# Kernel optimization log

Hardware: AMD Instinct MI355X
Metric: run time of the kernel (lower is better)

## Reference

```python
import jax, jax.numpy as jnp
import numpy as np
from jax.scipy.special import logsumexp

SIZE = 68          # DP length (self.size)
SSN = 8            # number of secondary-structure classes
C = SSN + 1        # states per step
S1 = SIZE + 1      # positions
BATCH = 256


def setup_inputs() -> dict:
    key = jax.random.key(0)
    k1, k2, k3, k4 = jax.random.split(key, 4)
    P = jax.random.normal(k1, (BATCH, 1, C, S1, S1), jnp.float32)
    Q = jax.random.normal(k2, (1, C, C, S1, S1), jnp.float32)
    pi = jax.random.normal(k3, (C,), jnp.float32)
    T = jnp.ones((1,), jnp.float32)
    ls = jax.random.randint(k4, (BATCH,), 0, S1, dtype=jnp.int32)
    return {"P": P, "Q": Q, "pi": pi, "T": T, "ls": ls}


def _max_alpha(P, Q, pi, T):
    # Viterbi-style max-plus recursion with logsumexp renormalization.
    b = P.shape[0]
    a0 = jnp.full((b, C, S1), -jnp.inf, P.dtype).at[:, :, 0].set(pi[None, :])
    n0 = logsumexp(a0, axis=(-1, -2), keepdims=True)      # (b,1,1)
    a0 = a0 - n0

    def step(carry, _):
        la, ln = carry                                    # (b,C,S1), (b,1,1)
        # broadcast sum over (b, c_prev, c_new, t_prev, t_new)
        M = P + T * Q + la[:, :, None, :, None]
        a = M.max(axis=(1, 3))                            # max over c_prev, t_prev -> (b,C,S1)
        n = ln + logsumexp(a, axis=(-1, -2), keepdims=True)
        a = a + ln - n
        return (a, n), (a, n)

    _, (a_seq, n_seq) = jax.lax.scan(step, (a0, n0), None, length=SIZE)
    a_all = jnp.concatenate([a0[None], a_seq], 0)          # (S1, b, C, S1) forward order
    n_all = jnp.concatenate([n0[None], n_seq], 0)          # (S1, b, 1, 1)
    # torch code stacks alpha REVERSED but norm in forward order, then adds
    alpha = a_all[::-1] + n_all
    return jnp.swapaxes(alpha, 0, 1)                       # (b, SIZE+1, C, S1)


def _backtrace(alpha, P, Q, T, ls):
    b = alpha.shape[0]
    Ps = P[:, 0]            # (b, C, S1, S1)
    Qs = Q[0]               # (C, C, S1, S1)
    bi = jnp.arange(b)
    c0 = jnp.full((b,), 3, jnp.int32)
    l0 = jnp.zeros((b,), jnp.int32)
    t0 = ls.astype(jnp.int32)

    def step(carry, a):
        c, l, t = carry
        Pterm = Ps[bi, c, :, t]                 # (b, S1)
        Qterm = Qs[c, :, :, t]                  # (b, C, S1)
        score = Pterm[:, None, :] + T * Qterm + a
        idx = jnp.argmax(score.reshape(b, -1), axis=-1).astype(jnp.int32)
        cn = idx // S1
        tn = idx % S1
        ln = tn - t
        return (cn, ln, tn), (cn, ln, tn)

    a_seq = jnp.swapaxes(alpha, 0, 1)[1:]       # (SIZE, b, C, S1)
    _, (cs, lss, ts) = jax.lax.scan(step, (c0, l0, t0), a_seq)
    c_all = jnp.concatenate([c0[None], cs], 0)[::-1]   # (SIZE+1, b)
    l_all = jnp.concatenate([l0[None], lss], 0)[::-1]
    t_all = jnp.concatenate([t0[None], ts], 0)[::-1]
    mp = jnp.swapaxes(jnp.stack([c_all, l_all, t_all], -1), 0, 1)  # (b, SIZE+1, 3)
    # shift length column: mp[:, :-1, 1] = mp[:, 1:, 1]; mp[:, -1, 1] = 0
    l_shift = jnp.concatenate([mp[:, 1:, 1], jnp.zeros((b, 1), jnp.int32)], 1)
    return mp.at[:, :, 1].set(l_shift)


def reference(P, Q, pi, T, ls):
    alpha = _max_alpha(P, Q, pi, T)
    max_pattern = _backtrace(alpha, P, Q, T, ls)
    return alpha, max_pattern
```

## Files before the change

### kernel.cpp

```cpp
#include <hip/hip_runtime.h>

#define C9     9
#define S1     69
#define JT     621
#define NBATCH 256
#define NSTEP  68
#define QJ     4761
#define QI     42849
#define BROW   42849
#define ALPHA_N (NBATCH*BROW)
#define QTFL   385664
#define NEGINF (-__builtin_inff())

typedef float float4u __attribute__((ext_vector_type(4), aligned(4)));

__global__ void qw_kernel(const float* __restrict__ Q, float* __restrict__ QW)
{
  const int bl = blockIdx.x;
  const int j = bl / S1, s = bl - j*S1;
  float* dst = QW + (size_t)bl*JT;
  const float* src = Q + (size_t)j*QJ + s*S1;
  for (int f = threadIdx.x; f < JT; f += 256){
    const int i = f / S1, t = f - i*S1;
    dst[f] = src[i*QJ + t];
  }
}

__global__ void qtrans_kernel(const float* __restrict__ Q, float* __restrict__ QT)
{
  __shared__ float tile[69*70];
  const int pl = blockIdx.x;
  const int c = pl / 9, i = pl - c*9;
  const float* src = Q + (size_t)pl*QJ;
  for (int f = threadIdx.x; f < QJ; f += 256){
    const int s = f / S1, t = f - s*S1;
    tile[s*70 + t] = src[f];
  }
  __syncthreads();
  float* dst = QT + (size_t)c*QI + i*S1;
  for (int f = threadIdx.x; f < QJ; f += 256){
    const int t = f / S1, s = f - t*S1;
    dst[t*JT + s] = tile[s*70 + t];
  }
}

template<int SI, int SS>
__device__ __forceinline__ float4u scan12(const float* __restrict__ qb,
                                          const float* __restrict__ pb,
                                          const float* __restrict__ laS,
                                          const float Tv)
{
#define LD(BUF, PV, S) { \
  const float* q_ = qb + (S)*SS; \
  _Pragma("unroll") \
  for (int i_ = 0; i_ < C9; ++i_) BUF[i_] = *(const float4u*)(q_ + i_*SI); \
  PV = *(const float4u*)(pb + (S)*S1); }
#define CM(BUF, PV, S) { \
  float r0=NEGINF, r1=NEGINF, r2=NEGINF, r3=NEGINF; \
  _Pragma("unroll") \
  for (int i_ = 0; i_ < C9; ++i_){ \
    const float lv_ = laS[i_*72 + (S)]; \
    r0 = fmaxf(r0, fmaf(Tv, BUF[i_].x, lv_)); \
    r1 = fmaxf(r1, fmaf(Tv, BUF[i_].y, lv_)); \
    r2 = fmaxf(r2, fmaf(Tv, BUF[i_].z, lv_)); \
    r3 = fmaxf(r3, fmaf(Tv, BUF[i_].w, lv_)); \
  } \
  acc.x = fmaxf(acc.x, PV.x + r0); acc.y = fmaxf(acc.y, PV.y + r1); \
  acc.z = fmaxf(acc.z, PV.z + r2); acc.w = fmaxf(acc.w, PV.w + r3); }

  float4u acc; acc.x = acc.y = acc.z = acc.w = NEGINF;
  float4u qA[C9], qB[C9], pA, pB;
  int s = 0;
  LD(qA, pA, s)
  for (; s + 2 < 12; s += 2){
    LD(qB, pB, s+1)
    CM(qA, pA, s)
    LD(qA, pA, s+2)
    CM(qB, pB, s+1)
  }
  LD(qB, pB, s+1)
  CM(qA, pA, s)
  CM(qB, pB, s+1)
  return acc;
#undef LD
#undef CM
}

__global__ __launch_bounds__(1024, 4) void mega_kernel(
    const float* __restrict__ P, const float* __restrict__ Q,
    const float* __restrict__ pi, const float* __restrict__ Tp,
    const int* __restrict__ ls, float* __restrict__ out,
    const float* __restrict__ QW, const float* __restrict__ QT, int wsmode)
{
  __shared__ __align__(16) float la[2][C9*72];
  __shared__ float part[5][162][4];
  __shared__ float red[16];
  __shared__ float m_sh[NSTEP+1], lse_sh[NSTEP+1], n_sh[NSTEP+1];
  __shared__ float sums_sh[NSTEP+1][3];
  __shared__ float sbest[16];
  __shared__ int   sidx[16];
  __shared__ int   sct[2];

  const int tid  = threadIdx.x;
  const int w    = tid >> 6;
  const int lane = tid & 63;
  const int b    = blockIdx.x;
  const bool act = tid < 972;
  const int gg   = act ? tid / 162 : 5;
  const int slot = act ? tid - gg*162 : 0;
  const int j    = slot / 18;
  const int tq   = slot - j*18;
  const int t0   = (tq < 17) ? 4*tq : 65;
  const int s_lo = (gg*23) >> 1;
  const float Tv = Tp[0];

  float* outb = out + (size_t)b*BROW;

  for (int e = tid; e < JT; e += 1024){
    const int i = e / S1, s = e - i*S1;
    const float v0 = (s == 0) ? pi[i] : NEGINF;
    outb[68*JT + e] = v0;
    la[0][i*72 + s] = v0;
  }
  if (tid == 0){
    float mx = pi[0];
    #pragma unroll
    for (int c = 1; c < C9; ++c) mx = fmaxf(mx, pi[c]);
    float sm = 0.f;
    #pragma unroll
    for (int c = 0; c < C9; ++c) sm += expf(pi[c] - mx);
    m_sh[0]   = mx;
    lse_sh[0] = mx + logf(sm);
  }
  __syncthreads();
  float mprev = m_sh[0];

  const bool useQW = (wsmode >= 1);
  const float* qw_b = QW + (size_t)j*QI + (size_t)s_lo*JT + t0;
  const float* qr_b = Q + (size_t)j*QJ + s_lo*S1 + t0;
  const float* p_b  = P + (size_t)(b*C9 + j)*QJ + s_lo*S1 + t0;

  int cur = 0;
  for (int k = 1; k <= NSTEP; ++k){
    const float* laS = la[cur] + s_lo;
    float4u acc;
    if (act){
      if (useQW) acc = scan12<S1, JT>(qw_b, p_b, laS, Tv);
      else       acc = scan12<QI, S1>(qr_b, p_b, laS, Tv);
      if (gg > 0){
        part[gg-1][slot][0] = acc.x; part[gg-1][slot][1] = acc.y;
        part[gg-1][slot][2] = acc.z; part[gg-1][slot][3] = acc.w;
      }
    }
    __syncthreads();

    float mval = NEGINF;
    float v0 = 0.f, v1 = 0.f, v2 = 0.f, v3 = 0.f;
    if (act && gg == 0){
      float c0 = acc.x, c1 = acc.y, c2 = acc.z, c3 = acc.w;
      #pragma unroll
      for (int g = 0; g < 5; ++g){
        c0 = fmaxf(c0, part[g][slot][0]);
        c1 = fmaxf(c1, part[g][slot][1]);
        c2 = fmaxf(c2, part[g][slot][2]);
        c3 = fmaxf(c3, part[g][slot][3]);
      }
      v0 = c0 - mprev; v1 = c1 - mprev; v2 = c2 - mprev; v3 = c3 - mprev;
      float* dst = outb + (size_t)(68-k)*JT + j*S1 + t0;
      if (tq < 17){
        float4u vv; vv.x = v0; vv.y = v1; vv.z = v2; vv.w = v3;
        *(float4u*)dst = vv;
        *(float4*)(&la[cur^1][j*72 + t0]) = make_float4(v0, v1, v2, v3);
        mval = fmaxf(fmaxf(v0, v1), fmaxf(v2, v3));
      } else {
        dst[3] = v3;
        la[cur^1][j*72 + 68] = v3;
        mval = v3;
      }
    }
    float mr = mval;
    #pragma unroll
    for (int o = 32; o >= 1; o >>= 1) mr = fmaxf(mr, __shfl_down(mr, o));
    if (lane == 0) red[w] = mr;
    __syncthreads();
    const float mA = fmaxf(fmaxf(red[0], red[1]), red[2]);
    if (act && gg == 0){
      float sv = (tq < 17)
        ? expf(v0 - mA) + expf(v1 - mA) + expf(v2 - mA) + expf(v3 - mA)
        : expf(v3 - mA);
      #pragma unroll
      for (int o = 32; o >= 1; o >>= 1) sv += __shfl_down(sv, o);
      if (lane == 0) sums_sh[k][w] = sv;
    }
    if (tid == 0) m_sh[k] = mA;
    mprev = mA;
    cur ^= 1;
  }
  __syncthreads();

  if (tid == 0){
    double dd = 0.0;
    for (int kk = 0; kk <= NSTEP; ++kk){
      float lse;
      if (kk == 0) lse = lse_sh[0];
      else lse = m_sh[kk] + logf(sums_sh[kk][0] + sums_sh[kk][1] + sums_sh[kk][2]);
      lse_sh[kk] = lse;
      n_sh[kk] = (float)((double)lse + dd);
      dd += (double)m_sh[kk];
    }
  }
  __syncthreads();

  for (int K = 0; K <= NSTEP; ++K){
    const float Cst = n_sh[K] - lse_sh[68-K];
    for (int e = tid; e < JT; e += 1024){
      float* r = outb + (size_t)K*JT + e;
      *r = fmaxf(*r + Cst, -3.0e38f);
    }
  }
  __syncthreads();

  {
    int c = 3, t2 = ls[b];
    float* mpb = out + (size_t)ALPHA_N + (size_t)b*(69*3);
    if (tid == 0){
      mpb[68*3+0] = 3.f; mpb[68*3+1] = 0.f; mpb[68*3+2] = (float)t2;
      mpb[67*3+1] = 0.f;
    }
    const bool vok = tid < JT;
    const int etid = vok ? tid : 0;
    const int im = etid / S1;
    const int sm = etid - im*S1;
    float av = vok ? outb[1*JT + tid] : NEGINF;
    for (int r = 1; r <= NSTEP; ++r){
      float avn = NEGINF;
      if (r < NSTEP && vok) avn = outb[(size_t)(r+1)*JT + tid];
      float best = NEGINF; int bidx = 0x7fffffff;
      if (vok){
        float qv;
        if (wsmode >= 2)      qv = QT[(size_t)c*QI + (size_t)t2*JT + tid];
        else if (wsmode == 1) qv = QW[(size_t)c*QI + (size_t)sm*JT + im*S1 + t2];
        else                  qv = Q[(size_t)c*QI + (size_t)im*QJ + sm*S1 + t2];
        const float pv = P[(size_t)(b*C9 + c)*QJ + sm*S1 + t2];
        best = (pv + Tv*qv) + av;
        bidx = tid;
      }
      #pragma unroll
      for (int o = 32; o >= 1; o >>= 1){
        const float ov = __shfl_down(best, o); const int oi = __shfl_down(bidx, o);
        if (ov > best || (ov == best && oi < bidx)){ best = ov; bidx = oi; }
      }
      if (lane == 0){ sbest[w] = best; sidx[w] = bidx; }
      __syncthreads();
      if (tid == 0){
        float bb = sbest[0]; int bi = sidx[0];
        #pragma unroll
        for (int q = 1; q < 16; ++q)
          if (sbest[q] > bb || (sbest[q] == bb && sidx[q] < bi)){
            bb = sbest[q]; bi = sidx[q];
          }
        const int cn = bi / S1, tn = bi - cn*S1;
        mpb[(68-r)*3 + 0] = (float)cn;
        mpb[(68-r)*3 + 2] = (float)tn;
        if (r <= 67) mpb[(67-r)*3 + 1] = (float)(tn - t2);
        sct[0] = cn; sct[1] = tn;
      }
      __syncthreads();
      c = sct[0]; t2 = sct[1];
      av = avn;
    }
  }
}

extern "C" void kernel_launch(void* const* d_in, const int* in_sizes, int n_in,
                              void* d_out, int out_size, void* d_ws, size_t ws_size,
                              hipStream_t stream)
{
  const float* P  = (const float*)d_in[0];
  const float* Q  = (const float*)d_in[1];
  const float* pi = (const float*)d_in[2];
  const float* T  = (const float*)d_in[3];
  const int*   ls = (const int*)d_in[4];

  float* out = (float*)d_out;

  int wsmode = 0; float* QW = nullptr; float* QT = nullptr;
  if (ws_size >= (size_t)QTFL*4){ wsmode = 1; QW = (float*)d_ws; }
  if (ws_size >= (size_t)2*QTFL*4){ wsmode = 2; QT = (float*)d_ws + QTFL; }

  if (wsmode >= 1) qw_kernel<<<JT, 256, 0, stream>>>(Q, QW);
  if (wsmode >= 2) qtrans_kernel<<<81, 256, 0, stream>>>(Q, QT);
  mega_kernel<<<NBATCH, 1024, 0, stream>>>(P, Q, pi, T, ls, out, QW, QT, wsmode);
}
```

Before: 2.223 ms.

## Process two batch elements per block to share Q loads across batches

Each block now handles two batch elements, so every Q tile loaded into registers in the inner max-plus scan serves both elements' alpha vectors. The grid is halved to 128 blocks, and all reductions, normalisation and backtrace are duplicated per element. This halves Q traffic per batch element and amortises barriers, at the cost of more registers, more shared memory and fewer blocks than the 256 CUs on MI355X, which may leave CUs idle.

Measured after the change: 2.760 ms. +24.1%, slower.

```diff
diff --git a/kernel.cpp b/kernel.cpp
--- a/kernel.cpp
+++ b/kernel.cpp
@@ -45,66 +45,78 @@
 }
 
 template<int SI, int SS>
-__device__ __forceinline__ float4u scan12(const float* __restrict__ qb,
-                                          const float* __restrict__ pb,
-                                          const float* __restrict__ laS,
-                                          const float Tv)
-{
-#define LD(BUF, PV, S) { \
+__device__ __forceinline__ void scan12x2(const float* __restrict__ qb,
+                                         const float* __restrict__ pb0,
+                                         const float* __restrict__ pb1,
+                                         const float* __restrict__ la0,
+                                         const float* __restrict__ la1,
+                                         const float Tv,
+                                         float4u& A0, float4u& A1)
+{
+#define LD(QB, P0, P1, S) { \
   const float* q_ = qb + (S)*SS; \
   _Pragma("unroll") \
-  for (int i_ = 0; i_ < C9; ++i_) BUF[i_] = *(const float4u*)(q_ + i_*SI); \
-  PV = *(const float4u*)(pb + (S)*S1); }
-#define CM(BUF, PV, S) { \
-  float r0=NEGINF, r1=NEGINF, r2=NEGINF, r3=NEGINF; \
+  for (int i_ = 0; i_ < C9; ++i_) QB[i_] = *(const float4u*)(q_ + i_*SI); \
+  P0 = *(const float4u*)(pb0 + (S)*S1); \
+  P1 = *(const float4u*)(pb1 + (S)*S1); }
+#define CM(QB, P0, P1, S) { \
+  float r00=NEGINF,r01=NEGINF,r02=NEGINF,r03=NEGINF; \
+  float r10=NEGINF,r11=NEGINF,r12=NEGINF,r13=NEGINF; \
   _Pragma("unroll") \
   for (int i_ = 0; i_ < C9; ++i_){ \
-    const float lv_ = laS[i_*72 + (S)]; \
-    r0 = fmaxf(r0, fmaf(Tv, BUF[i_].x, lv_)); \
-    r1 = fmaxf(r1, fmaf(Tv, BUF[i_].y, lv_)); \
-    r2 = fmaxf(r2, fmaf(Tv, BUF[i_].z, lv_)); \
-    r3 = fmaxf(r3, fmaf(Tv, BUF[i_].w, lv_)); \
+    const float l0_ = la0[i_*72 + (S)]; \
+    const float l1_ = la1[i_*72 + (S)]; \
+    r00 = fmaxf(r00, fmaf(Tv, QB[i_].x, l0_)); \
+    r01 = fmaxf(r01, fmaf(Tv, QB[i_].y, l0_)); \
+    r02 = fmaxf(r02, fmaf(Tv, QB[i_].z, l0_)); \
+    r03 = fmaxf(r03, fmaf(Tv, QB[i_].w, l0_)); \
+    r10 = fmaxf(r10, fmaf(Tv, QB[i_].x, l1_)); \
+    r11 = fmaxf(r11, fmaf(Tv, QB[i_].y, l1_)); \
+    r12 = fmaxf(r12, fmaf(Tv, QB[i_].z, l1_)); \
+    r13 = fmaxf(r13, fmaf(Tv, QB[i_].w, l1_)); \
   } \
-  acc.x = fmaxf(acc.x, PV.x + r0); acc.y = fmaxf(acc.y, PV.y + r1); \
-  acc.z = fmaxf(acc.z, PV.z + r2); acc.w = fmaxf(acc.w, PV.w + r3); }
-
-  float4u acc; acc.x = acc.y = acc.z = acc.w = NEGINF;
-  float4u qA[C9], qB[C9], pA, pB;
+  A0.x = fmaxf(A0.x, P0.x + r00); A0.y = fmaxf(A0.y, P0.y + r01); \
+  A0.z = fmaxf(A0.z, P0.z + r02); A0.w = fmaxf(A0.w, P0.w + r03); \
+  A1.x = fmaxf(A1.x, P1.x + r10); A1.y = fmaxf(A1.y, P1.y + r11); \
+  A1.z = fmaxf(A1.z, P1.z + r12); A1.w = fmaxf(A1.w, P1.w + r13); }
+
+  float4u qA[C9], qB[C9], pA0, pA1, pB0, pB1;
   int s = 0;
-  LD(qA, pA, s)
+  LD(qA, pA0, pA1, s)
   for (; s + 2 < 12; s += 2){
-    LD(qB, pB, s+1)
-    CM(qA, pA, s)
-    LD(qA, pA, s+2)
-    CM(qB, pB, s+1)
-  }
-  LD(qB, pB, s+1)
-  CM(qA, pA, s)
-  CM(qB, pB, s+1)
-  return acc;
+    LD(qB, pB0, pB1, s+1)
+    CM(qA, pA0, pA1, s)
+    LD(qA, pA0, pA1, s+2)
+    CM(qB, pB0, pB1, s+1)
+  }
+  LD(qB, pB0, pB1, s+1)
+  CM(qA, pA0, pA1, s)
+  CM(qB, pB0, pB1, s+1)
 #undef LD
 #undef CM
 }
 
-__global__ __launch_bounds__(1024, 4) void mega_kernel(
+__global__ __attribute__((amdgpu_waves_per_eu(4, 4)))
+__launch_bounds__(1024) void mega_kernel(
     const float* __restrict__ P, const float* __restrict__ Q,
     const float* __restrict__ pi, const float* __restrict__ Tp,
     const int* __restrict__ ls, float* __restrict__ out,
     const float* __restrict__ QW, const float* __restrict__ QT, int wsmode)
 {
-  __shared__ __align__(16) float la[2][C9*72];
-  __shared__ float part[5][162][4];
-  __shared__ float red[16];
-  __shared__ float m_sh[NSTEP+1], lse_sh[NSTEP+1], n_sh[NSTEP+1];
-  __shared__ float sums_sh[NSTEP+1][3];
-  __shared__ float sbest[16];
-  __shared__ int   sidx[16];
-  __shared__ int   sct[2];
+  __shared__ __align__(16) float la[2][2][C9*72];
+  __shared__ __align__(16) float part[5][162][2][4];
+  __shared__ float red[2][16];
+  __shared__ float m_sh[2][NSTEP+1], lse_sh[2][NSTEP+1], n_sh[2][NSTEP+1];
+  __shared__ float sums_sh[2][NSTEP+1][3];
+  __shared__ float sbest[2][16];
+  __shared__ int   sidx[2][16];
+  __shared__ int   sct[4];
 
   const int tid  = threadIdx.x;
   const int w    = tid >> 6;
   const int lane = tid & 63;
-  const int b    = blockIdx.x;
+  const int b0   = blockIdx.x * 2;
+  const int b1   = b0 + 1;
   const bool act = tid < 972;
   const int gg   = act ? tid / 162 : 5;
   const int slot = act ? tid - gg*162 : 0;
@@ -114,13 +126,16 @@
   const int s_lo = (gg*23) >> 1;
   const float Tv = Tp[0];
 
-  float* outb = out + (size_t)b*BROW;
+  float* out0 = out + (size_t)b0*BROW;
+  float* out1 = out + (size_t)b1*BROW;
 
   for (int e = tid; e < JT; e += 1024){
     const int i = e / S1, s = e - i*S1;
     const float v0 = (s == 0) ? pi[i] : NEGINF;
-    outb[68*JT + e] = v0;
-    la[0][i*72 + s] = v0;
+    out0[68*JT + e] = v0;
+    out1[68*JT + e] = v0;
+    la[0][0][i*72 + s] = v0;
+    la[1][0][i*72 + s] = v0;
   }
   if (tid == 0){
     float mx = pi[0];
@@ -129,145 +144,217 @@
     float sm = 0.f;
     #pragma unroll
     for (int c = 0; c < C9; ++c) sm += expf(pi[c] - mx);
-    m_sh[0]   = mx;
-    lse_sh[0] = mx + logf(sm);
-  }
-  __syncthreads();
-  float mprev = m_sh[0];
+    m_sh[0][0] = mx;            m_sh[1][0] = mx;
+    lse_sh[0][0] = mx + logf(sm); lse_sh[1][0] = mx + logf(sm);
+  }
+  __syncthreads();
+  float mprev0 = m_sh[0][0];
+  float mprev1 = m_sh[1][0];
 
   const bool useQW = (wsmode >= 1);
   const float* qw_b = QW + (size_t)j*QI + (size_t)s_lo*JT + t0;
   const float* qr_b = Q + (size_t)j*QJ + s_lo*S1 + t0;
-  const float* p_b  = P + (size_t)(b*C9 + j)*QJ + s_lo*S1 + t0;
+  const float* p0_b = P + (size_t)(b0*C9 + j)*QJ + s_lo*S1 + t0;
+  const float* p1_b = p0_b + QI;
 
   int cur = 0;
   for (int k = 1; k <= NSTEP; ++k){
-    const float* laS = la[cur] + s_lo;
-    float4u acc;
+    const float* laS0 = la[0][cur] + s_lo;
+    const float* laS1 = la[1][cur] + s_lo;
+    float4u A0, A1;
+    A0.x=A0.y=A0.z=A0.w=NEGINF; A1.x=A1.y=A1.z=A1.w=NEGINF;
     if (act){
-      if (useQW) acc = scan12<S1, JT>(qw_b, p_b, laS, Tv);
-      else       acc = scan12<QI, S1>(qr_b, p_b, laS, Tv);
+      if (useQW) scan12x2<S1, JT>(qw_b, p0_b, p1_b, laS0, laS1, Tv, A0, A1);
+      else       scan12x2<QI, S1>(qr_b, p0_b, p1_b, laS0, laS1, Tv, A0, A1);
       if (gg > 0){
-        part[gg-1][slot][0] = acc.x; part[gg-1][slot][1] = acc.y;
-        part[gg-1][slot][2] = acc.z; part[gg-1][slot][3] = acc.w;
+        *(float4u*)(&part[gg-1][slot][0][0]) = A0;
+        *(float4u*)(&part[gg-1][slot][1][0]) = A1;
       }
     }
     __syncthreads();
 
-    float mval = NEGINF;
-    float v0 = 0.f, v1 = 0.f, v2 = 0.f, v3 = 0.f;
+    float mval0 = NEGINF, mval1 = NEGINF;
+    float v00=0.f, v01=0.f, v02=0.f, v03=0.f;
+    float v10=0.f, v11=0.f, v12=0.f, v13=0.f;
     if (act && gg == 0){
-      float c0 = acc.x, c1 = acc.y, c2 = acc.z, c3 = acc.w;
+      float c00=A0.x, c01=A0.y, c02=A0.z, c03=A0.w;
+      float c10=A1.x, c11=A1.y, c12=A1.z, c13=A1.w;
       #pragma unroll
       for (int g = 0; g < 5; ++g){
-        c0 = fmaxf(c0, part[g][slot][0]);
-        c1 = fmaxf(c1, part[g][slot][1]);
-        c2 = fmaxf(c2, part[g][slot][2]);
-        c3 = fmaxf(c3, part[g][slot][3]);
-      }
-      v0 = c0 - mprev; v1 = c1 - mprev; v2 = c2 - mprev; v3 = c3 - mprev;
-      float* dst = outb + (size_t)(68-k)*JT + j*S1 + t0;
+        c00 = fmaxf(c00, part[g][slot][0][0]);
+        c01 = fmaxf(c01, part[g][slot][0][1]);
+        c02 = fmaxf(c02, part[g][slot][0][2]);
+        c03 = fmaxf(c03, part[g][slot][0][3]);
+        c10 = fmaxf(c10, part[g][slot][1][0]);
+        c11 = fmaxf(c11, part[g][slot][1][1]);
+        c12 = fmaxf(c12, part[g][slot][1][2]);
+        c13 = fmaxf(c13, part[g][slot][1][3]);
+      }
+      v00 = c00 - mprev0; v01 = c01 - mprev0; v02 = c02 - mprev0; v03 = c03 - mprev0;
+      v10 = c10 - mprev1; v11 = c11 - mprev1; v12 = c12 - mprev1; v13 = c13 - mprev1;
+      float* d0 = out0 + (size_t)(68-k)*JT + j*S1 + t0;
+      float* d1 = out1 + (size_t)(68-k)*JT + j*S1 + t0;
       if (tq < 17){
-        float4u vv; vv.x = v0; vv.y = v1; vv.z = v2; vv.w = v3;
-        *(float4u*)dst = vv;
-        *(float4*)(&la[cur^1][j*72 + t0]) = make_float4(v0, v1, v2, v3);
-        mval = fmaxf(fmaxf(v0, v1), fmaxf(v2, v3));
+        float4u w0; w0.x=v00; w0.y=v01; w0.z=v02; w0.w=v03;
+        float4u w1; w1.x=v10; w1.y=v11; w1.z=v12; w1.w=v13;
+        *(float4u*)d0 = w0;
+        *(float4u*)d1 = w1;
+        *(float4*)(&la[0][cur^1][j*72 + t0]) = make_float4(v00, v01, v02, v03);
+        *(float4*)(&la[1][cur^1][j*72 + t0]) = make_float4(v10, v11, v12, v13);
+        mval0 = fmaxf(fmaxf(v00, v01), fmaxf(v02, v03));
+        mval1 = fmaxf(fmaxf(v10, v11), fmaxf(v12, v13));
       } else {
-        dst[3] = v3;
-        la[cur^1][j*72 + 68] = v3;
-        mval = v3;
-      }
-    }
-    float mr = mval;
+        d0[3] = v03;  d1[3] = v13;
+        la[0][cur^1][j*72 + 68] = v03;
+        la[1][cur^1][j*72 + 68] = v13;
+        mval0 = v03;  mval1 = v13;
+      }
+    }
+    float mr0 = mval0, mr1 = mval1;
     #pragma unroll
-    for (int o = 32; o >= 1; o >>= 1) mr = fmaxf(mr, __shfl_down(mr, o));
-    if (lane == 0) red[w] = mr;
+    for (int o = 32; o >= 1; o >>= 1){
+      mr0 = fmaxf(mr0, __shfl_down(mr0, o));
+      mr1 = fmaxf(mr1, __shfl_down(mr1, o));
+    }
+    if (lane == 0){ red[0][w] = mr0; red[1][w] = mr1; }
     __syncthreads();
-    const float mA = fmaxf(fmaxf(red[0], red[1]), red[2]);
+    const float mA0 = fmaxf(fmaxf(red[0][0], red[0][1]), red[0][2]);
+    const float mA1 = fmaxf(fmaxf(red[1][0], red[1][1]), red[1][2]);
     if (act && gg == 0){
-      float sv = (tq < 17)
-        ? expf(v0 - mA) + expf(v1 - mA) + expf(v2 - mA) + expf(v3 - mA)
-        : expf(v3 - mA);
+      float sv0, sv1;
+      if (tq < 17){
+        sv0 = expf(v00-mA0) + expf(v01-mA0) + expf(v02-mA0) + expf(v03-mA0);
+        sv1 = expf(v10-mA1) + expf(v11-mA1) + expf(v12-mA1) + expf(v13-mA1);
+      } else {
+        sv0 = expf(v03-mA0);
+        sv1 = expf(v13-mA1);
+      }
       #pragma unroll
-      for (int o = 32; o >= 1; o >>= 1) sv += __shfl_down(sv, o);
-      if (lane == 0) sums_sh[k][w] = sv;
-    }
-    if (tid == 0) m_sh[k] = mA;
-    mprev = mA;
+      for (int o = 32; o >= 1; o >>= 1){
+        sv0 += __shfl_down(sv0, o);
+        sv1 += __shfl_down(sv1, o);
+      }
+      if (lane == 0){ sums_sh[0][k][w] = sv0; sums_sh[1][k][w] = sv1; }
+    }
+    if (tid == 0){ m_sh[0][k] = mA0; m_sh[1][k] = mA1; }
+    mprev0 = mA0; mprev1 = mA1;
     cur ^= 1;
   }
   __syncthreads();
 
   if (tid == 0){
-    double dd = 0.0;
+    double d0 = 0.0, d1 = 0.0;
     for (int kk = 0; kk <= NSTEP; ++kk){
-      float lse;
-      if (kk == 0) lse = lse_sh[0];
-      else lse = m_sh[kk] + logf(sums_sh[kk][0] + sums_sh[kk][1] + sums_sh[kk][2]);
-      lse_sh[kk] = lse;
-      n_sh[kk] = (float)((double)lse + dd);
-      dd += (double)m_sh[kk];
+      float l0, l1;
+      if (kk == 0){ l0 = lse_sh[0][0]; l1 = lse_sh[1][0]; }
+      else {
+        l0 = m_sh[0][kk] + logf(sums_sh[0][kk][0] + sums_sh[0][kk][1] + sums_sh[0][kk][2]);
+        l1 = m_sh[1][kk] + logf(sums_sh[1][kk][0] + sums_sh[1][kk][1] + sums_sh[1][kk][2]);
+      }
+      lse_sh[0][kk] = l0;  lse_sh[1][kk] = l1;
+      n_sh[0][kk] = (float)((double)l0 + d0);
+      n_sh[1][kk] = (float)((double)l1 + d1);
+      d0 += (double)m_sh[0][kk];
+      d1 += (double)m_sh[1][kk];
     }
   }
   __syncthreads();
 
   for (int K = 0; K <= NSTEP; ++K){
-    const float Cst = n_sh[K] - lse_sh[68-K];
+    const float C0 = n_sh[0][K] - lse_sh[0][68-K];
+    const float C1 = n_sh[1][K] - lse_sh[1][68-K];
     for (int e = tid; e < JT; e += 1024){
-      float* r = outb + (size_t)K*JT + e;
-      *r = fmaxf(*r + Cst, -3.0e38f);
+      float* r0 = out0 + (size_t)K*JT + e;
+      float* r1 = out1 + (size_t)K*JT + e;
+      *r0 = fmaxf(*r0 + C0, -3.0e38f);
+      *r1 = fmaxf(*r1 + C1, -3.0e38f);
     }
   }
   __syncthreads();
 
   {
-    int c = 3, t2 = ls[b];
-    float* mpb = out + (size_t)ALPHA_N + (size_t)b*(69*3);
+    int c0 = 3, t20 = ls[b0];
+    int c1 = 3, t21 = ls[b1];
+    float* mpb0 = out + (size_t)ALPHA_N + (size_t)b0*(69*3);
+    float* mpb1 = out + (size_t)ALPHA_N + (size_t)b1*(69*3);
     if (tid == 0){
-      mpb[68*3+0] = 3.f; mpb[68*3+1] = 0.f; mpb[68*3+2] = (float)t2;
-      mpb[67*3+1] = 0.f;
+      mpb0[68*3+0] = 3.f; mpb0[68*3+1] = 0.f; mpb0[68*3+2] = (float)t20;
+      mpb0[67*3+1] = 0.f;
+      mpb1[68*3+0] = 3.f; mpb1[68*3+1] = 0.f; mpb1[68*3+2] = (float)t21;
+      mpb1[67*3+1] = 0.f;
     }
     const bool vok = tid < JT;
     const int etid = vok ? tid : 0;
     const int im = etid / S1;
     const int sm = etid - im*S1;
-    float av = vok ? outb[1*JT + tid] : NEGINF;
+    float av0 = vok ? out0[1*JT + tid] : NEGINF;
+    float av1 = vok ? out1[1*JT + tid] : NEGINF;
     for (int r = 1; r <= NSTEP; ++r){
-      float avn = NEGINF;
-      if (r < NSTEP && vok) avn = outb[(size_t)(r+1)*JT + tid];
-      float best = NEGINF; int bidx = 0x7fffffff;
+      float avn0 = NEGINF, avn1 = NEGINF;
+      if (r < NSTEP && vok){
+        avn0 = out0[(size_t)(r+1)*JT + tid];
+        avn1 = out1[(size_t)(r+1)*JT + tid];
+      }
+      float best0 = NEGINF, best1 = NEGINF;
+      int bi0 = 0x7fffffff, bi1 = 0x7fffffff;
       if (vok){
-        float qv;
-        if (wsmode >= 2)      qv = QT[(size_t)c*QI + (size_t)t2*JT + tid];
-        else if (wsmode == 1) qv = QW[(size_t)c*QI + (size_t)sm*JT + im*S1 + t2];
-        else                  qv = Q[(size_t)c*QI + (size_t)im*QJ + sm*S1 + t2];
-        const float pv = P[(size_t)(b*C9 + c)*QJ + sm*S1 + t2];
-        best = (pv + Tv*qv) + av;
-        bidx = tid;
+        float q0, q1;
+        if (wsmode >= 2){
+          q0 = QT[(size_t)c0*QI + (size_t)t20*JT + tid];
+          q1 = QT[(size_t)c1*QI + (size_t)t21*JT + tid];
+        } else if (wsmode == 1){
+          q0 = QW[(size_t)c0*QI + (size_t)sm*JT + im*S1 + t20];
+          q1 = QW[(size_t)c1*QI + (size_t)sm*JT + im*S1 + t21];
+        } else {
+          q0 = Q[(size_t)c0*QI + (size_t)im*QJ + sm*S1 + t20];
+          q1 = Q[(size_t)c1*QI + (size_t)im*QJ + sm*S1 + t21];
+        }
+        const float pv0 = P[(size_t)(b0*C9 + c0)*QJ + sm*S1 + t20];
+        const float pv1 = P[(size_t)(b1*C9 + c1)*QJ + sm*S1 + t21];
+        best0 = (pv0 + Tv*q0) + av0; bi0 = tid;
+        best1 = (pv1 + Tv*q1) + av1; bi1 = tid;
       }
       #pragma unroll
       for (int o = 32; o >= 1; o >>= 1){
-        const float ov = __shfl_down(best, o); const int oi = __shfl_down(bidx, o);
-        if (ov > best || (ov == best && oi < bidx)){ best = ov; bidx = oi; }
-      }
-      if (lane == 0){ sbest[w] = best; sidx[w] = bidx; }
+        const float ov0 = __shfl_down(best0, o); const int oi0 = __shfl_down(bi0, o);
+        if (ov0 > best0 || (ov0 == best0 && oi0 < bi0)){ best0 = ov0; bi0 = oi0; }
+        const float ov1 = __shfl_down(best1, o); const int oi1 = __shfl_down(bi1, o);
+        if (ov1 > best1 || (ov1 == best1 && oi1 < bi1)){ best1 = ov1; bi1 = oi1; }
+      }
+      if (lane == 0){
+        sbest[0][w] = best0; sidx[0][w] = bi0;
+        sbest[1][w] = best1; sidx[1][w] = bi1;
+      }
       __syncthreads();
       if (tid == 0){
-        float bb = sbest[0]; int bi = sidx[0];
+        float bb = sbest[0][0]; int bi = sidx[0][0];
         #pragma unroll
         for (int q = 1; q < 16; ++q)
-          if (sbest[q] > bb || (sbest[q] == bb && sidx[q] < bi)){
-            bb = sbest[q]; bi = sidx[q];
+          if (sbest[0][q] > bb || (sbest[0][q] == bb && sidx[0][q] < bi)){
+            bb = sbest[0][q]; bi = sidx[0][q];
           }
-        const int cn = bi / S1, tn = bi - cn*S1;
-        mpb[(68-r)*3 + 0] = (float)cn;
-        mpb[(68-r)*3 + 2] = (float)tn;
-        if (r <= 67) mpb[(67-r)*3 + 1] = (float)(tn - t2);
+        int cn = bi / S1, tn = bi - (bi/S1)*S1;
+        mpb0[(68-r)*3 + 0] = (float)cn;
+        mpb0[(68-r)*3 + 2] = (float)tn;
+        if (r <= 67) mpb0[(67-r)*3 + 1] = (float)(tn - t20);
         sct[0] = cn; sct[1] = tn;
+
+        bb = sbest[1][0]; bi = sidx[1][0];
+        #pragma unroll
+        for (int q = 1; q < 16; ++q)
+          if (sbest[1][q] > bb || (sbest[1][q] == bb && sidx[1][q] < bi)){
+            bb = sbest[1][q]; bi = sidx[1][q];
+          }
+        cn = bi / S1; tn = bi - (bi/S1)*S1;
+        mpb1[(68-r)*3 + 0] = (float)cn;
+        mpb1[(68-r)*3 + 2] = (float)tn;
+        if (r <= 67) mpb1[(67-r)*3 + 1] = (float)(tn - t21);
+        sct[2] = cn; sct[3] = tn;
       }
       __syncthreads();
-      c = sct[0]; t2 = sct[1];
-      av = avn;
+      c0 = sct[0]; t20 = sct[1];
+      c1 = sct[2]; t21 = sct[3];
+      av0 = avn0; av1 = avn1;
     }
   }
 }
@@ -290,5 +377,5 @@
 
   if (wsmode >= 1) qw_kernel<<<JT, 256, 0, stream>>>(Q, QW);
   if (wsmode >= 2) qtrans_kernel<<<81, 256, 0, stream>>>(Q, QT);
-  mega_kernel<<<NBATCH, 1024, 0, stream>>>(P, Q, pi, T, ls, out, QW, QT, wsmode);
-}
+  mega_kernel<<<NBATCH/2, 1024, 0, stream>>>(P, Q, pi, T, ls, out, QW, QT, wsmode);
+}
```
